# Kernel optimization log

Hardware: AMD Instinct MI355X
Metric: run time of the kernel (lower is better)

Reference implementation:

```python
import jax, jax.numpy as jnp
import numpy as np

CUTOFF = 5.0
CUTOFF_ANGLE = 3.5
N = 25000
E = 800000
EA = 300000
T = 1600000
NBASIS = 8          # default radial basis size (bessel)
NBASIS_ANG = 8
DIM = 256
DIM_SRC = 64
DIM_DST = 32
DIM_ANGLE = 8
NMAX_ANGLE = 4
SPECIES_DIM = 16
NSPEC = 50


def bessel_basis(r, rc, n):
    # sin(k*pi*r/rc)/r Bessel-type radial basis, k=1..n  -> [E, n]
    x = r[:, None]
    k = jnp.arange(1, n + 1, dtype=r.dtype)[None, :] * (np.pi / rc)
    return jnp.sqrt(2.0 / rc) * jnp.sin(k * x) / x


def tssr2(x):
    # two-sided smooth square-root activation (identity inside |x|<=1)
    ax = jnp.abs(x)
    return jnp.where(ax <= 1.0, x, jnp.sign(x) * (2.0 * jnp.sqrt(jnp.maximum(ax, 1.0)) - 1.0))


def setup_inputs() -> dict:
    key = jax.random.key(0)
    ks = jax.random.split(key, 24)
    species = jax.random.randint(ks[0], (N,), 1, 17)
    edge_src = jax.random.randint(ks[1], (E,), 0, N)
    edge_dst = jax.random.randint(ks[2], (E,), 0, N)
    distances = 0.5 + jax.random.uniform(ks[3], (E,)) * (CUTOFF - 0.5)
    switch = 0.5 + 0.5 * jnp.cos(np.pi * distances / CUTOFF)
    angles = jax.random.uniform(ks[4], (T,)) * np.pi
    angle_src = jax.random.randint(ks[5], (T,), 0, EA)
    angle_dst = jax.random.randint(ks[6], (T,), 0, EA)
    central_atom = jax.random.randint(ks[7], (T,), 0, N)
    distances_angle = 0.5 + jax.random.uniform(ks[8], (EA,)) * (CUTOFF_ANGLE - 0.5)
    switch_angle = 0.5 + 0.5 * jnp.cos(np.pi * distances_angle / CUTOFF_ANGLE)
    s = lambda k, sh, scale: jax.random.normal(k, sh, jnp.float32) * scale
    din0 = SPECIES_DIM + DIM_SRC + NBASIS * DIM_DST + (NMAX_ANGLE + 1) * DIM_ANGLE  # 376
    din1 = DIM + DIM_SRC + NBASIS * DIM_DST + (NMAX_ANGLE + 1) * DIM_ANGLE          # 616
    return {
        'species': species, 'edge_src': edge_src, 'edge_dst': edge_dst,
        'distances': distances, 'switch': switch,
        'angles': angles, 'angle_src': angle_src, 'angle_dst': angle_dst,
        'central_atom': central_atom, 'distances_angle': distances_angle,
        'switch_angle': switch_angle,
        'species_table': s(ks[9], (NSPEC, SPECIES_DIM), 1.0),
        'W_si0': s(ks[10], (SPECIES_DIM, DIM_SRC + DIM_DST), SPECIES_DIM ** -0.5),
        'W_si1': s(ks[11], (DIM, DIM_SRC + DIM_DST), DIM ** -0.5),
        'W_da0': s(ks[12], (NBASIS_ANG, DIM_ANGLE), NBASIS_ANG ** -0.5),
        'W_da1': s(ks[13], (NBASIS_ANG, DIM_ANGLE), NBASIS_ANG ** -0.5),
        'W_mix0': s(ks[14], (din0, DIM), din0 ** -0.5),
        'b_mix0': jnp.zeros((DIM,), jnp.float32),
        'W_mix1': s(ks[15], (din1, DIM), din1 ** -0.5),
        'b_mix1': jnp.zeros((DIM,), jnp.float32),
    }


def reference(species, edge_src, edge_dst, distances, switch, angles, angle_src,
              angle_dst, central_atom, distances_angle, switch_angle,
              species_table, W_si0, W_si1, W_da0, W_da1,
              W_mix0, b_mix0, W_mix1, b_mix1):
    n_atoms = species.shape[0]
    # species encoding (learned/random table lookup)
    xi = species_table[species]                                   # [N, 16]
    # radial embeddings, smoothly switched at cutoff
    rb = bessel_basis(distances, CUTOFF, NBASIS) * switch[:, None]            # [E, 8]
    rba = bessel_basis(distances_angle, CUTOFF_ANGLE, NBASIS_ANG) * switch_angle[:, None]  # [EA, 8]
    # fourier angular features cos(n*theta), n=0..nmax_angle
    nvec = jnp.arange(NMAX_ANGLE + 1, dtype=angles.dtype)[None, :]
    xa = jnp.cos(nvec * angles[:, None])                          # [T, 5]
    for W_si, W_da, W_mix, b_mix in ((W_si0, W_da0, W_mix0, b_mix0),
                                     (W_si1, W_da1, W_mix1, b_mix1)):
        s = xi @ W_si                                             # [N, 96]
        si, si_dst = s[:, :DIM_SRC], s[:, DIM_SRC:]
        # radial message passing: outer(radial_basis, neighbor features) -> scatter-add
        mij = (rb[:, :, None] * si_dst[edge_dst][:, None, :]).reshape(rb.shape[0], -1)  # [E, 256]
        mi = jax.ops.segment_sum(mij, edge_src, num_segments=n_atoms)                   # [N, 256]
        # angular triplet features: pairwise vectors combined per angle
        da = rba @ W_da                                           # [EA, 8]
        dij = da[angle_src] * da[angle_dst]                       # [T, 8]
        ang = (xa[:, :, None] * dij[:, None, :]).reshape(xa.shape[0], -1)               # [T, 40]
        ami = jax.ops.segment_sum(ang, central_atom, num_segments=n_atoms)              # [N, 40]
        # mixing network + tssr2 mixing activation, residual when shapes match
        ei = jnp.concatenate([xi, si, mi, ami], axis=-1)
        dxi = tssr2(ei @ W_mix + b_mix)
        xi = xi + dxi if xi.shape[-1] == dxi.shape[-1] else dxi
    return xi
```

## Files before the change

### kernel.cpp

```cpp
#include <hip/hip_runtime.h>
#include <hip/hip_bf16.h>

typedef __hip_bfloat16 bf16;
typedef __bf16 bf8 __attribute__((ext_vector_type(8)));
typedef float  f4  __attribute__((ext_vector_type(4)));

#define N_ATOMS 25000
#define NE      800000
#define NEA     300000
#define NT      1600000
#define APB     64
#define NBUK    ((N_ATOMS + APB - 1) / APB)

#define DIN0  376
#define DIN1  616
#define DINP0 384
#define DINP1 640

#define EBLK ((NE + 4095) / 4096)
#define TBLK ((NT + 4095) / 4096)

#define NFRAG0 ((DINP0 / 32) * 16 * 64)
#define NFRAG1 ((DINP1 / 32) * 16 * 64)
#define NFRAGS (8 * 6 * 64)

#define S0BLK ((N_ATOMS * 120 + 255) / 256)
#define DABLK ((NEA + 255) / 256)

#define MIBLK ((N_ATOMS + 1) / 2)

__device__ __forceinline__ float tssr2f(float x) {
    float ax = fabsf(x);
    return (ax <= 1.f) ? x : copysignf(2.f * __builtin_sqrtf(ax) - 1.f, x);
}

__device__ __forceinline__ unsigned short f2bf_rn(float v) {
    unsigned int b = __float_as_uint(v);
    b += 0x7FFF + ((b >> 16) & 1);
    return (unsigned short)(b >> 16);
}
__device__ __forceinline__ float bf2f(unsigned short u) {
    return __uint_as_float(((unsigned int)u) << 16);
}

__global__ __launch_bounds__(256) void k_bcount(const int* __restrict__ esrc,
                                                const int* __restrict__ cat,
                                                int* __restrict__ ebcnt,
                                                int* __restrict__ tbcnt) {
    __shared__ int h[NBUK];
    int t = threadIdx.x;
    for (int b = t; b < NBUK; b += 256) h[b] = 0;
    __syncthreads();
    bool isE = blockIdx.x < EBLK;
    const int* key = isE ? esrc : cat;
    int n = isE ? NE : NT;
    int base = (isE ? blockIdx.x : (blockIdx.x - EBLK)) * 4096;
#pragma unroll
    for (int k = 0; k < 16; k++) {
        int idx = base + k * 256 + t;
        if (idx < n) atomicAdd(&h[key[idx] >> 6], 1);
    }
    __syncthreads();
    int* g = isE ? ebcnt : tbcnt;
    for (int b = t; b < NBUK; b += 256)
        if (h[b]) atomicAdd(&g[b], h[b]);
}

__global__ __launch_bounds__(512) void k_scanB(const int* cnt0, int* off0, int* cur0,
                                               int* aoff0,
                                               const int* cnt1, int* off1, int* cur1,
                                               int* aoff1) {
    const int* cnt = blockIdx.x ? cnt1 : cnt0;
    int* off  = blockIdx.x ? off1 : off0;
    int* cur  = blockIdx.x ? cur1 : cur0;
    int* aoff = blockIdx.x ? aoff1 : aoff0;
    int nelem = blockIdx.x ? NT : NE;
    __shared__ int sh[512];
    int t = threadIdx.x;
    int v = (t < NBUK) ? cnt[t] : 0;
    sh[t] = v;
    __syncthreads();
    for (int d = 1; d < 512; d <<= 1) {
        int a = (t >= d) ? sh[t - d] : 0;
        __syncthreads();
        sh[t] += a;
        __syncthreads();
    }
    int excl = sh[t] - v;
    if (t <= NBUK) { off[t] = excl; if (t < NBUK) cur[t] = excl; }
    if (t == 0) aoff[N_ATOMS] = nelem;
}

__global__ __launch_bounds__(512) void k_binA2(const float* __restrict__ eA,
                                               const float* __restrict__ eB,
                                               const int* __restrict__ eC,
                                               const int* __restrict__ ekey,
                                               int* __restrict__ egcur,
                                               float4* __restrict__ ebuk,
                                               const float* __restrict__ tA,
                                               const int* __restrict__ tB,
                                               const int* __restrict__ tC,
                                               const int* __restrict__ tkey,
                                               int* __restrict__ tgcur,
                                               float4* __restrict__ tbuk) {
    __shared__ int cnt[NBUK];
    __shared__ int rbase[NBUK];
    int t = threadIdx.x;
    for (int b = t; b < NBUK; b += 512) cnt[b] = 0;
    __syncthreads();
    bool isE = blockIdx.x < EBLK;
    const int* key = isE ? ekey : tkey;
    int n = isE ? NE : NT;
    int* gcur = isE ? egcur : tgcur;
    float4* buk = isE ? ebuk : tbuk;
    int base = (isE ? blockIdx.x : (blockIdx.x - EBLK)) * 4096;
    float4 pay[8];
    int bk[8], off[8];
#pragma unroll
    for (int k = 0; k < 8; k++) {
        int idx = base + k * 512 + t;
        bk[k] = -1;
        if (idx < n) {
            float4 p;
            if (isE) {
                p.x = eA[idx];
                p.y = eB[idx];
                p.z = __int_as_float(eC[idx]);
            } else {
                p.x = __cosf(tA[idx]);
                p.y = __int_as_float(tB[idx]);
                p.z = __int_as_float(tC[idx]);
            }
            int ky = key[idx];
            p.w = __int_as_float(ky);
            pay[k] = p;
            bk[k] = ky >> 6;
            off[k] = atomicAdd(&cnt[bk[k]], 1);
        }
    }
    __syncthreads();
    for (int b = t; b < NBUK; b += 512)
        if (cnt[b]) rbase[b] = atomicAdd(&gcur[b], cnt[b]);
    __syncthreads();
#pragma unroll
    for (int k = 0; k < 8; k++)
        if (bk[k] >= 0) buk[rbase[bk[k]] + off[k]] = pay[k];
}

__global__ __launch_bounds__(256) void k_binB2(const int* __restrict__ ebkoff,
                                               const float4* __restrict__ ebuk,
                                               float* __restrict__ erb,
                                               int* __restrict__ edi,
                                               int* __restrict__ eoff,
                                               const int* __restrict__ tbkoff,
                                               const float4* __restrict__ tbuk,
                                               float4* __restrict__ tfin,
                                               int* __restrict__ toff) {
    bool isE = blockIdx.x < NBUK;
    int b = isE ? blockIdx.x : (blockIdx.x - NBUK);
    const int* bkoff = isE ? ebkoff : tbkoff;
    const float4* buk = isE ? ebuk : tbuk;
    int* aoff = isE ? eoff : toff;
    int lo = b * APB;
    int hi = min(lo + APB, N_ATOMS);
    __shared__ int cnt[APB];
    __shared__ int cur[APB];
    int t = threadIdx.x;
    if (t < APB) cnt[t] = 0;
    __syncthreads();
    int pbeg = bkoff[b], pend = bkoff[b + 1];
    for (int p = pbeg + t; p < pend; p += 256) {
        int a = __float_as_int(((const float*)(buk + p))[3]);
        atomicAdd(&cnt[a - lo], 1);
    }
    __syncthreads();
    if (t == 0) {
        int run = pbeg;
        for (int k = 0; k < hi - lo; k++) {
            cur[k] = run;
            aoff[lo + k] = run;
            run += cnt[k];
        }
    }
    __syncthreads();
    for (int p = pbeg + t; p < pend; p += 256) {
        float4 pay = buk[p];
        int a = __float_as_int(pay.w);
        int slot = atomicAdd(&cur[a - lo], 1);
        if (isE) {
            float d = pay.x, s = pay.y;
            float q = 0.6324555320f * s / d;
            float r[8];
#pragma unroll
            for (int n = 0; n < 8; n++)
                r[n] = q * __sinf((n + 1) * 0.6283185307f * d);
            *(float4*)&erb[(size_t)slot * 8]     = make_float4(r[0], r[1], r[2], r[3]);
            *(float4*)&erb[(size_t)slot * 8 + 4] = make_float4(r[4], r[5], r[6], r[7]);
            edi[slot] = __float_as_int(pay.z);
        } else {
            tfin[slot] = pay;
        }
    }
}

__device__ __forceinline__ void wprep_one(const float* __restrict__ W, bf8* __restrict__ Wf,
                                          int K, int N, int ntiles, int f) {
    int lane = f & 63;
    int ft = f >> 6;
    int tile = ft % ntiles;
    int chunk = ft / ntiles;
    int n = tile * 16 + (lane & 15);
    int kb = chunk * 32 + (lane >> 4) * 8;
    bf8 v;
#pragma unroll
    for (int j = 0; j < 8; j++) {
        int k = kb + j;
        v[j] = (__bf16)((k < K) ? W[k * N + n] : 0.f);
    }
    Wf[f] = v;
}

__global__ __launch_bounds__(256) void k_wprep3(const float* __restrict__ W0, bf8* __restrict__ Wf0,
                                                const float* __restrict__ W1, bf8* __restrict__ Wf1,
                                                const float* __restrict__ WS, bf8* __restrict__ WfS) {
    int f = blockIdx.x * 256 + threadIdx.x;
    if (f < NFRAG0) {
        wprep_one(W0, Wf0, DIN0, 256, 16, f);
    } else if (f < NFRAG0 + NFRAG1) {
        wprep_one(W1, Wf1, DIN1, 256, 16, f - NFRAG0);
    } else if (f < NFRAG0 + NFRAG1 + NFRAGS) {
        wprep_one(WS, WfS, 256, 96, 6, f - NFRAG0 - NFRAG1);
    }
}

__global__ __launch_bounds__(256) void k_pre(const int* __restrict__ sp,
                                             const float* __restrict__ table,
                                             const float* __restrict__ W,
                                             float* __restrict__ ei0,
                                             float* __restrict__ sd,
                                             const float* __restrict__ dist,
                                             const float* __restrict__ sw,
                                             const float* __restrict__ Wda0,
                                             const float* __restrict__ Wda1,
                                             unsigned short* __restrict__ dah0,
                                             unsigned short* __restrict__ dah1) {
    if ((int)blockIdx.x < S0BLK) {
        int idx = blockIdx.x * 256 + threadIdx.x;
        if (idx >= N_ATOMS * 120) return;
        int i = idx / 120;
        int c = idx - i * 120;
        if (c >= 112) {
            ei0[(size_t)i * DINP0 + 376 + (c - 112)] = 0.f;
            return;
        }
        int s = sp[i];
        if (c < 16) {
            ei0[(size_t)i * DINP0 + c] = table[s * 16 + c];
        } else {
            int cc = c - 16;
            float acc = 0.f;
#pragma unroll
            for (int k = 0; k < 16; k++)
                acc += table[s * 16 + k] * W[k * 96 + cc];
            if (cc < 64) ei0[(size_t)i * DINP0 + 16 + cc] = acc;
            else         sd[i * 32 + cc - 64]             = acc;
        }
    } else {
        int e = (blockIdx.x - S0BLK) * 256 + threadIdx.x;
        if (e >= NEA) return;
        float d = dist[e];
        float s = sw[e];
        float rb[8];
#pragma unroll
        for (int n = 0; n < 8; n++)
            rb[n] = 0.7559289460f * __sinf((n + 1) * 0.8975979010f * d) / d * s;
        unsigned short h0[8], h1[8];
#pragma unroll
        for (int c = 0; c < 8; c++) {
            float a0 = 0.f, a1 = 0.f;
#pragma unroll
            for (int n = 0; n < 8; n++) {
                a0 += rb[n] * Wda0[n * 8 + c];
                a1 += rb[n] * Wda1[n * 8 + c];
            }
            h0[c] = f2bf_rn(a0);
            h1[c] = f2bf_rn(a1);
        }
        *(uint4*)&dah0[e * 8] = *(uint4*)h0;
        *(uint4*)&dah1[e * 8] = *(uint4*)h1;
    }
}

__global__ __launch_bounds__(256) void k_s1(const float* __restrict__ ei1,
                                            const bf8* __restrict__ Wf,
                                            float* __restrict__ ei1o,
                                            float* __restrict__ sd) {
    __shared__ __align__(16) __bf16 Asg[4][64][8];
    int t = threadIdx.x;
    int w = t >> 6, lane = t & 63;
    int a0 = blockIdx.x * 64;

    int satom = a0 + (t >> 2);
    int k8 = (t & 3) * 8;
    const float* arow = &ei1[(size_t)satom * DINP1 + k8];
    bool aok = satom < N_ATOMS;
    int dw = (t >> 2) >> 4;
    int dl = ((t >> 2) & 15) | ((t & 3) << 4);
    __bf16* adst = &Asg[dw][dl][0];

    f4 acc[6];
#pragma unroll
    for (int j = 0; j < 6; j++) {
        f4 z = {0.f, 0.f, 0.f, 0.f};
        acc[j] = z;
    }

    for (int ch = 0; ch < 8; ch++) {
        float4 v0 = make_float4(0.f, 0.f, 0.f, 0.f);
        float4 v1 = make_float4(0.f, 0.f, 0.f, 0.f);
        if (aok) {
            v0 = *(const float4*)(arow + ch * 32);
            v1 = *(const float4*)(arow + ch * 32 + 4);
        }
        __syncthreads();
        adst[0] = (__bf16)v0.x; adst[1] = (__bf16)v0.y;
        adst[2] = (__bf16)v0.z; adst[3] = (__bf16)v0.w;
        adst[4] = (__bf16)v1.x; adst[5] = (__bf16)v1.y;
        adst[6] = (__bf16)v1.z; adst[7] = (__bf16)v1.w;
        __syncthreads();
        bf8 afr = *(const bf8*)&Asg[w][lane][0];
        const bf8* wp = &Wf[(ch * 6) * 64 + lane];
#pragma unroll
        for (int tn = 0; tn < 6; tn++) {
            bf8 b = wp[tn * 64];
            acc[tn] = __builtin_amdgcn_mfma_f32_16x16x32_bf16(afr, b, acc[tn], 0, 0, 0);
        }
    }

    int nlo = lane & 15, q = lane >> 4;
#pragma unroll
    for (int r = 0; r < 4; r++) {
        int atom = a0 + w * 16 + q * 4 + r;
        if (atom < N_ATOMS) {
#pragma unroll
            for (int tn = 0; tn < 6; tn++) {
                int col = tn * 16 + nlo;
                float v = acc[tn][r];
                if (col < 64) ei1o[(size_t)atom * DINP1 + 256 + col] = v;
                else          sd[atom * 32 + col - 64] = v;
            }
        }
    }
    for (int z = t; z < 64 * 24; z += 256) {
        int za = a0 + z / 24;
        if (za < N_ATOMS) ei1o[(size_t)za * DINP1 + 616 + z % 24] = 0.f;
    }
}

__device__ __forceinline__ void ami_win(const float4 twA, const unsigned short* __restrict__ dah,
                                        int lim, int jj, int c,
                                        float& a0, float& a1, float& a2, float& a3, float& a4) {
    int gmax = (lim + 7) >> 3;
    float sc = 0.f; unsigned short dA = 0, dB = 0;
    {
        sc = __shfl(twA.x, jj, 64);
        int ea = __float_as_int(__shfl(twA.y, jj, 64));
        int eb = __float_as_int(__shfl(twA.z, jj, 64));
        dA = dah[ea * 8 + c];
        dB = dah[eb * 8 + c];
    }
    for (int g = 0; g < gmax; g++) {
        float scN = 0.f; unsigned short dAN = 0, dBN = 0;
        if (g + 1 < gmax) {
            int sl = (g + 1) * 8 + jj;
            scN = __shfl(twA.x, sl, 64);
            int ea = __float_as_int(__shfl(twA.y, sl, 64));
            int eb = __float_as_int(__shfl(twA.z, sl, 64));
            dAN = dah[ea * 8 + c];
            dBN = dah[eb * 8 + c];
        }
        float dij = bf2f(dA) * bf2f(dB);
        dij = (g * 8 + jj < lim) ? dij : 0.f;
        float c1 = sc;
        float c2 = __builtin_fmaf(2.f * c1, c1, -1.f);
        float c3 = __builtin_fmaf(2.f * c1, c2, -c1);
        float c4 = __builtin_fmaf(2.f * c1, c3, -c2);
        a0 += dij;
        a1 = __builtin_fmaf(c1, dij, a1);
        a2 = __builtin_fmaf(c2, dij, a2);
        a3 = __builtin_fmaf(c3, dij, a3);
        a4 = __builtin_fmaf(c4, dij, a4);
        if (g + 1 < gmax) { sc = scN; dA = dAN; dB = dBN; }
    }
}

__global__ __launch_bounds__(256) void k_seg(const int* __restrict__ eoff,
                                             const float* __restrict__ erb,
                                             const int* __restrict__ edi,
                                             const float* __restrict__ sd,
                                             float* __restrict__ mo, int mstride,
                                             const int* __restrict__ toff,
                                             const float4* __restrict__ tpay,
                                             const unsigned short* __restrict__ dah,
                                             float* __restrict__ ao, int astride) {
    __shared__ float4 smi[2][64];
    __shared__ float  sam[2][5][8];
    int t = threadIdx.x;
    int wv = t >> 6, l = t & 63;
    int slot = wv >> 1;
    int p    = wv & 1;

    if ((int)blockIdx.x < MIBLK) {
        int i = blockIdx.x * 2 + slot;
        bool valid = (i < N_ATOMS);
        int beg = 0, end = 0;
        if (valid) { beg = eoff[i]; end = eoff[i + 1]; }
        int cnt = end - beg;
        int n = l >> 3, cb = (l & 7) * 4;
        float4 acc = make_float4(0.f, 0.f, 0.f, 0.f);

        if (cnt > 0) {
            int nG = (cnt + 7) >> 3;
            int h0 = (nG + 1) >> 1;
            int gbeg = p ? h0 : 0;
            int gend = p ? nG : h0;
            if (cnt <= 64) {
                int eWin = edi[beg + min(l, cnt - 1)];
                int cmax = end * 8 - 1;
                if (gbeg < gend) {
                    float cA = erb[min((beg + gbeg * 8) * 8 + l, cmax)];
                    for (int g = gbeg; g < gend; g++) {
                        int e8 = g * 8;
                        float4 v[8];
#pragma unroll
                        for (int j = 0; j < 8; j++) {
                            int eid = __shfl(eWin, e8 + j, 64);
                            v[j] = *(const float4*)&sd[eid * 32 + cb];
                        }
                        float cB = 0.f;
                        if (g + 1 < gend) cB = erb[min((beg + e8 + 8) * 8 + l, cmax)];
#pragma unroll
                        for (int j = 0; j < 8; j++) {
                            float r_ = __shfl(cA, j * 8 + n, 64);
                            r_ = (e8 + j < cnt) ? r_ : 0.f;
                            acc.x += r_ * v[j].x; acc.y += r_ * v[j].y;
                            acc.z += r_ * v[j].z; acc.w += r_ * v[j].w;
                        }
                        if (g + 1 < gend) cA = cB;
                    }
                }
            } else {
                const float* rp = erb + (size_t)beg * 8 + n;
                const int*   dp = edi + beg;
                for (int g = gbeg; g < gend; g++) {
                    int e8 = g * 8;
                    int m = cnt - e8;
#pragma unroll
                    for (int j = 0; j < 8; j++) {
                        int jj = min(j, m - 1);
                        float rb = rp[(e8 + jj) * 8];
                        int di = dp[e8 + jj];
                        if (j >= m) rb = 0.f;
                        float4 v = *(const float4*)&sd[di * 32 + cb];
                        acc.x += rb * v.x; acc.y += rb * v.y;
                        acc.z += rb * v.z; acc.w += rb * v.w;
                    }
                }
            }
        }

        if (p == 1) smi[slot][l] = acc;
        __syncthreads();
        if (valid && p == 0) {
            float4 o = smi[slot][l];
            acc.x += o.x; acc.y += o.y; acc.z += o.z; acc.w += o.w;
            *(float4*)&mo[(size_t)i * mstride + l * 4] = acc;
        }
    } else {
        int i = ((int)blockIdx.x - MIBLK) * 2 + slot;
        bool valid = (i < N_ATOMS);
        int beg = 0, end = 0;
        if (valid) { beg = toff[i]; end = toff[i + 1]; }
        int cnt = end - beg;
        int jj = l >> 3, c = l & 7;
        float a0 = 0.f, a1 = 0.f, a2 = 0.f, a3 = 0.f, a4 = 0.f;

        if (cnt > 0) {
            if (cnt <= 128) {
                int nG = (cnt + 7) >> 3;
                int h0 = (nG + 1) >> 1;
                int tb = p ? h0 * 8 : 0;
                int te = p ? cnt : min(h0 * 8, cnt);
                int mycnt = te - tb;
                if (mycnt > 0) {
                    float4 twA = tpay[beg + tb + min(l, mycnt - 1)];
                    ami_win(twA, dah, mycnt, jj, c, a0, a1, a2, a3, a4);
                }
            } else {
                int nW = (cnt + 63) >> 6;
                for (int W = p; W < nW; W += 2) {
                    int wbase = W * 64;
                    int rem = cnt - wbase;
                    int lim = min(rem, 64);
                    float4 twA = tpay[beg + wbase + min(l, rem - 1)];
                    ami_win(twA, dah, lim, jj, c, a0, a1, a2, a3, a4);
                }
            }
        }

#pragma unroll
        for (int msk = 8; msk <= 32; msk <<= 1) {
            a0 += __shfl_xor(a0, msk, 64);
            a1 += __shfl_xor(a1, msk, 64);
            a2 += __shfl_xor(a2, msk, 64);
            a3 += __shfl_xor(a3, msk, 64);
            a4 += __shfl_xor(a4, msk, 64);
        }
        if (p == 1 && l < 8) {
            sam[slot][0][l] = a0; sam[slot][1][l] = a1; sam[slot][2][l] = a2;
            sam[slot][3][l] = a3; sam[slot][4][l] = a4;
        }
        __syncthreads();
        if (valid && p == 0 && l < 8) {
            a0 += sam[slot][0][l]; a1 += sam[slot][1][l]; a2 += sam[slot][2][l];
            a3 += sam[slot][3][l]; a4 += sam[slot][4][l];
            float* o = &ao[(size_t)i * astride + c];
            o[0]  = a0;
            o[8]  = a1;
            o[16] = a2;
            o[24] = a3;
            o[32] = a4;
        }
    }
}

template <int LAYER>
__global__ __launch_bounds__(256) void k_gemm(const float* __restrict__ ei,
                                              const bf8* __restrict__ Wf,
                                              const float* __restrict__ bias,
                                              const float* __restrict__ skip,
                                              float* __restrict__ out) {
    constexpr int DINP = (LAYER == 0) ? DINP0 : DINP1;
    constexpr int NCH = DINP / 32;
    __shared__ __align__(16) __bf16 Asg[2][64][8];
    int t = threadIdx.x;
    int w = t >> 6, lane = t & 63;
    int a0 = blockIdx.x * 32;

    int f  = t * 4;
    int tA = f >> 9;
    int al = (f >> 3) & 63;
    int j0 = f & 7;
    int sm = al & 15, sq = al >> 4;
    int ga = a0 + tA * 16 + sm;
    const float* arow = &ei[(size_t)ga * DINP + sq * 8 + j0];
    __bf16* adst = &Asg[0][0][0] + f;
    bool aok = (ga < N_ATOMS);

    f4 acc[2][4];
#pragma unroll
    for (int i = 0; i < 2; i++)
#pragma unroll
        for (int j = 0; j < 4; j++) {
            f4 z = {0.f, 0.f, 0.f, 0.f};
            acc[i][j] = z;
        }

    for (int ch = 0; ch < NCH; ch++) {
        float4 v = make_float4(0.f, 0.f, 0.f, 0.f);
        if (aok) v = *(const float4*)(arow + ch * 32);
        __syncthreads();
        adst[0] = (__bf16)v.x; adst[1] = (__bf16)v.y;
        adst[2] = (__bf16)v.z; adst[3] = (__bf16)v.w;
        __syncthreads();
        bf8 afr0 = *(const bf8*)&Asg[0][lane][0];
        bf8 afr1 = *(const bf8*)&Asg[1][lane][0];
        const bf8* wp = &Wf[(ch * 16 + w * 4) * 64 + lane];
#pragma unroll
        for (int tn = 0; tn < 4; tn++) {
            bf8 b = wp[tn * 64];
            acc[0][tn] = __builtin_amdgcn_mfma_f32_16x16x32_bf16(afr0, b, acc[0][tn], 0, 0, 0);
            acc[1][tn] = __builtin_amdgcn_mfma_f32_16x16x32_bf16(afr1, b, acc[1][tn], 0, 0, 0);
        }
    }

    int nlo = lane & 15, q = lane >> 4;
#pragma unroll
    for (int tA2 = 0; tA2 < 2; tA2++) {
#pragma unroll
        for (int r = 0; r < 4; r++) {
            int atom = a0 + tA2 * 16 + q * 4 + r;
            if (atom < N_ATOMS) {
#pragma unroll
                for (int tn = 0; tn < 4; tn++) {
                    int col = w * 64 + tn * 16 + nlo;
                    float vv = tssr2f(acc[tA2][tn][r] + bias[col]);
                    if (LAYER == 0) {
                        out[(size_t)atom * DINP1 + col] = vv;
                    } else {
                        out[(size_t)atom * 256 + col] = vv + skip[(size_t)atom * DINP1 + col];
                    }
                }
            }
        }
    }
}

extern "C" void kernel_launch(void* const* d_in, const int* in_sizes, int n_in,
                              void* d_out, int out_size, void* d_ws, size_t ws_size,
                              hipStream_t stream) {
    const int*   species     = (const int*)d_in[0];
    const int*   edge_src    = (const int*)d_in[1];
    const int*   edge_dst    = (const int*)d_in[2];
    const float* distances   = (const float*)d_in[3];
    const float* sw          = (const float*)d_in[4];
    const float* angles      = (const float*)d_in[5];
    const int*   angle_src   = (const int*)d_in[6];
    const int*   angle_dst   = (const int*)d_in[7];
    const int*   central     = (const int*)d_in[8];
    const float* dist_a      = (const float*)d_in[9];
    const float* sw_a        = (const float*)d_in[10];
    const float* table       = (const float*)d_in[11];
    const float* W_si0       = (const float*)d_in[12];
    const float* W_si1       = (const float*)d_in[13];
    const float* W_da0       = (const float*)d_in[14];
    const float* W_da1       = (const float*)d_in[15];
    const float* W_mix0      = (const float*)d_in[16];
    const float* b_mix0      = (const float*)d_in[17];
    const float* W_mix1      = (const float*)d_in[18];
    const float* b_mix1      = (const float*)d_in[19];
    float* out = (float*)d_out;

    char* p = (char*)d_ws;
    auto alloc = [&](size_t bytes) {
        char* r = p;
        p += (bytes + 255) & ~(size_t)255;
        return (void*)r;
    };
    float*  ei0  = (float*)alloc((size_t)N_ATOMS * DINP0 * 4);
    float*  ei1  = (float*)alloc((size_t)N_ATOMS * DINP1 * 4);
    float*  sd   = (float*)alloc((size_t)N_ATOMS * 32 * 4);
    unsigned short* dah0 = (unsigned short*)alloc((size_t)NEA * 8 * 2);
    unsigned short* dah1 = (unsigned short*)alloc((size_t)NEA * 8 * 2);
    float*  erbf = (float*)alloc((size_t)NE * 8 * 4);
    int*    edi  = (int*)alloc((size_t)NE * 4);
    float4* tpay = (float4*)alloc((size_t)NT * 16);
    bf8*    Wf0  = (bf8*)alloc((size_t)NFRAG0 * 16);
    bf8*    Wf1  = (bf8*)alloc((size_t)NFRAG1 * 16);
    bf8*    WfS1 = (bf8*)alloc((size_t)NFRAGS * 16);
    int* eoff   = (int*)alloc((size_t)(N_ATOMS + 1) * 4);
    int* toff   = (int*)alloc((size_t)(N_ATOMS + 1) * 4);
    int* bcnt   = (int*)alloc((size_t)2 * NBUK * 4);
    int* ebkoff = (int*)alloc((size_t)(NBUK + 1) * 4);
    int* tbkoff = (int*)alloc((size_t)(NBUK + 1) * 4);
    int* gce    = (int*)alloc((size_t)NBUK * 4);
    int* gct    = (int*)alloc((size_t)NBUK * 4);
    (void)ws_size;
    int* ebcnt = bcnt;
    int* tbcnt = bcnt + NBUK;

    float4* tbuk = (float4*)ei1;
    float4* ebuk = (float4*)((char*)ei1 + (size_t)NT * 16);

    hipMemsetAsync(bcnt, 0, (size_t)2 * NBUK * 4, stream);

    k_wprep3<<<(NFRAG0 + NFRAG1 + NFRAGS + 255) / 256, 256, 0, stream>>>(
        W_mix0, Wf0, W_mix1, Wf1, W_si1, WfS1);

    k_bcount<<<EBLK + TBLK, 256, 0, stream>>>(edge_src, central, ebcnt, tbcnt);
    k_scanB<<<2, 512, 0, stream>>>(ebcnt, ebkoff, gce, eoff, tbcnt, tbkoff, gct, toff);

    k_binA2<<<EBLK + TBLK, 512, 0, stream>>>(
        distances, sw, edge_dst, edge_src, gce, ebuk,
        angles, angle_src, angle_dst, central, gct, tbuk);
    k_binB2<<<2 * NBUK, 256, 0, stream>>>(
        ebkoff, ebuk, erbf, edi, eoff,
        tbkoff, tbuk, tpay, toff);

    k_pre<<<S0BLK + DABLK, 256, 0, stream>>>(
        species, table, W_si0, ei0, sd,
        dist_a, sw_a, W_da0, W_da1, dah0, dah1);

    int gemm_grid = (N_ATOMS + 31) / 32;

    k_seg<<<2 * MIBLK, 256, 0, stream>>>(eoff, erbf, edi, sd, ei0 + 80, DINP0,
                                         toff, tpay, dah0, ei0 + 336, DINP0);
    k_gemm<0><<<gemm_grid, 256, 0, stream>>>(ei0, Wf0, b_mix0, nullptr, ei1);

    k_s1<<<(N_ATOMS + 63) / 64, 256, 0, stream>>>(ei1, WfS1, ei1, sd);
    k_seg<<<2 * MIBLK, 256, 0, stream>>>(eoff, erbf, edi, sd, ei1 + 320, DINP1,
                                         toff, tpay, dah1, ei1 + 576, DINP1);
    k_gemm<1><<<gemm_grid, 256, 0, stream>>>(ei1, Wf1, b_mix1, ei1, out);
}
```

Before: 417.6 us.

## Store intermediate per-atom feature buffers in bf16 instead of fp32

The concatenated per-atom feature buffers (ei0, ei1) are now written and read as bf16 rather than fp32. The seg, pre and s1 kernels round their outputs to bf16, and the GEMM kernels copy the bf16 words straight into shared memory instead of loading floats and converting. This is meant to roughly halve the memory traffic on these large intermediates, since the GEMM already consumed them as bf16. The k_seg block ordering is also swapped so that triplet (angular) blocks come before the radial message blocks, and the bucket scratch space is re-aliased into the smaller buffers. The trade-off is that the residual skip connection and stored features lose precision through bf16 rounding.

After: 412.2 us. Within noise of the previous version (-1.3%).

```diff
diff --git a/kernel.cpp b/kernel.cpp
--- a/kernel.cpp
+++ b/kernel.cpp
@@ -236,7 +236,7 @@
 __global__ __launch_bounds__(256) void k_pre(const int* __restrict__ sp,
                                              const float* __restrict__ table,
                                              const float* __restrict__ W,
-                                             float* __restrict__ ei0,
+                                             unsigned short* __restrict__ ei0,
                                              float* __restrict__ sd,
                                              const float* __restrict__ dist,
                                              const float* __restrict__ sw,
@@ -250,19 +250,19 @@
         int i = idx / 120;
         int c = idx - i * 120;
         if (c >= 112) {
-            ei0[(size_t)i * DINP0 + 376 + (c - 112)] = 0.f;
+            ei0[(size_t)i * DINP0 + 376 + (c - 112)] = 0;
             return;
         }
         int s = sp[i];
         if (c < 16) {
-            ei0[(size_t)i * DINP0 + c] = table[s * 16 + c];
+            ei0[(size_t)i * DINP0 + c] = f2bf_rn(table[s * 16 + c]);
         } else {
             int cc = c - 16;
             float acc = 0.f;
 #pragma unroll
             for (int k = 0; k < 16; k++)
                 acc += table[s * 16 + k] * W[k * 96 + cc];
-            if (cc < 64) ei0[(size_t)i * DINP0 + 16 + cc] = acc;
+            if (cc < 64) ei0[(size_t)i * DINP0 + 16 + cc] = f2bf_rn(acc);
             else         sd[i * 32 + cc - 64]             = acc;
         }
     } else {
@@ -291,9 +291,9 @@
     }
 }
 
-__global__ __launch_bounds__(256) void k_s1(const float* __restrict__ ei1,
+__global__ __launch_bounds__(256) void k_s1(const unsigned short* __restrict__ ei1,
                                             const bf8* __restrict__ Wf,
-                                            float* __restrict__ ei1o,
+                                            unsigned short* __restrict__ ei1o,
                                             float* __restrict__ sd) {
     __shared__ __align__(16) __bf16 Asg[4][64][8];
     int t = threadIdx.x;
@@ -302,7 +302,7 @@
 
     int satom = a0 + (t >> 2);
     int k8 = (t & 3) * 8;
-    const float* arow = &ei1[(size_t)satom * DINP1 + k8];
+    const unsigned short* arow = &ei1[(size_t)satom * DINP1 + k8];
     bool aok = satom < N_ATOMS;
     int dw = (t >> 2) >> 4;
     int dl = ((t >> 2) & 15) | ((t & 3) << 4);
@@ -316,17 +316,10 @@
     }
 
     for (int ch = 0; ch < 8; ch++) {
-        float4 v0 = make_float4(0.f, 0.f, 0.f, 0.f);
-        float4 v1 = make_float4(0.f, 0.f, 0.f, 0.f);
-        if (aok) {
-            v0 = *(const float4*)(arow + ch * 32);
-            v1 = *(const float4*)(arow + ch * 32 + 4);
-        }
-        __syncthreads();
-        adst[0] = (__bf16)v0.x; adst[1] = (__bf16)v0.y;
-        adst[2] = (__bf16)v0.z; adst[3] = (__bf16)v0.w;
-        adst[4] = (__bf16)v1.x; adst[5] = (__bf16)v1.y;
-        adst[6] = (__bf16)v1.z; adst[7] = (__bf16)v1.w;
+        uint4 v = make_uint4(0, 0, 0, 0);
+        if (aok) v = *(const uint4*)(arow + ch * 32);
+        __syncthreads();
+        *(uint4*)adst = v;
         __syncthreads();
         bf8 afr = *(const bf8*)&Asg[w][lane][0];
         const bf8* wp = &Wf[(ch * 6) * 64 + lane];
@@ -346,14 +339,14 @@
             for (int tn = 0; tn < 6; tn++) {
                 int col = tn * 16 + nlo;
                 float v = acc[tn][r];
-                if (col < 64) ei1o[(size_t)atom * DINP1 + 256 + col] = v;
+                if (col < 64) ei1o[(size_t)atom * DINP1 + 256 + col] = f2bf_rn(v);
                 else          sd[atom * 32 + col - 64] = v;
             }
         }
     }
     for (int z = t; z < 64 * 24; z += 256) {
         int za = a0 + z / 24;
-        if (za < N_ATOMS) ei1o[(size_t)za * DINP1 + 616 + z % 24] = 0.f;
+        if (za < N_ATOMS) ei1o[(size_t)za * DINP1 + 616 + z % 24] = 0;
     }
 }
 
@@ -398,11 +391,11 @@
                                              const float* __restrict__ erb,
                                              const int* __restrict__ edi,
                                              const float* __restrict__ sd,
-                                             float* __restrict__ mo, int mstride,
+                                             unsigned short* __restrict__ mo, int mstride,
                                              const int* __restrict__ toff,
                                              const float4* __restrict__ tpay,
                                              const unsigned short* __restrict__ dah,
-                                             float* __restrict__ ao, int astride) {
+                                             unsigned short* __restrict__ ao, int astride) {
     __shared__ float4 smi[2][64];
     __shared__ float  sam[2][5][8];
     int t = threadIdx.x;
@@ -412,72 +405,6 @@
 
     if ((int)blockIdx.x < MIBLK) {
         int i = blockIdx.x * 2 + slot;
-        bool valid = (i < N_ATOMS);
-        int beg = 0, end = 0;
-        if (valid) { beg = eoff[i]; end = eoff[i + 1]; }
-        int cnt = end - beg;
-        int n = l >> 3, cb = (l & 7) * 4;
-        float4 acc = make_float4(0.f, 0.f, 0.f, 0.f);
-
-        if (cnt > 0) {
-            int nG = (cnt + 7) >> 3;
-            int h0 = (nG + 1) >> 1;
-            int gbeg = p ? h0 : 0;
-            int gend = p ? nG : h0;
-            if (cnt <= 64) {
-                int eWin = edi[beg + min(l, cnt - 1)];
-                int cmax = end * 8 - 1;
-                if (gbeg < gend) {
-                    float cA = erb[min((beg + gbeg * 8) * 8 + l, cmax)];
-                    for (int g = gbeg; g < gend; g++) {
-                        int e8 = g * 8;
-                        float4 v[8];
-#pragma unroll
-                        for (int j = 0; j < 8; j++) {
-                            int eid = __shfl(eWin, e8 + j, 64);
-                            v[j] = *(const float4*)&sd[eid * 32 + cb];
-                        }
-                        float cB = 0.f;
-                        if (g + 1 < gend) cB = erb[min((beg + e8 + 8) * 8 + l, cmax)];
-#pragma unroll
-                        for (int j = 0; j < 8; j++) {
-                            float r_ = __shfl(cA, j * 8 + n, 64);
-                            r_ = (e8 + j < cnt) ? r_ : 0.f;
-                            acc.x += r_ * v[j].x; acc.y += r_ * v[j].y;
-                            acc.z += r_ * v[j].z; acc.w += r_ * v[j].w;
-                        }
-                        if (g + 1 < gend) cA = cB;
-                    }
-                }
-            } else {
-                const float* rp = erb + (size_t)beg * 8 + n;
-                const int*   dp = edi + beg;
-                for (int g = gbeg; g < gend; g++) {
-                    int e8 = g * 8;
-                    int m = cnt - e8;
-#pragma unroll
-                    for (int j = 0; j < 8; j++) {
-                        int jj = min(j, m - 1);
-                        float rb = rp[(e8 + jj) * 8];
-                        int di = dp[e8 + jj];
-                        if (j >= m) rb = 0.f;
-                        float4 v = *(const float4*)&sd[di * 32 + cb];
-                        acc.x += rb * v.x; acc.y += rb * v.y;
-                        acc.z += rb * v.z; acc.w += rb * v.w;
-                    }
-                }
-            }
-        }
-
-        if (p == 1) smi[slot][l] = acc;
-        __syncthreads();
-        if (valid && p == 0) {
-            float4 o = smi[slot][l];
-            acc.x += o.x; acc.y += o.y; acc.z += o.z; acc.w += o.w;
-            *(float4*)&mo[(size_t)i * mstride + l * 4] = acc;
-        }
-    } else {
-        int i = ((int)blockIdx.x - MIBLK) * 2 + slot;
         bool valid = (i < N_ATOMS);
         int beg = 0, end = 0;
         if (valid) { beg = toff[i]; end = toff[i + 1]; }
@@ -524,22 +451,91 @@
         if (valid && p == 0 && l < 8) {
             a0 += sam[slot][0][l]; a1 += sam[slot][1][l]; a2 += sam[slot][2][l];
             a3 += sam[slot][3][l]; a4 += sam[slot][4][l];
-            float* o = &ao[(size_t)i * astride + c];
-            o[0]  = a0;
-            o[8]  = a1;
-            o[16] = a2;
-            o[24] = a3;
-            o[32] = a4;
+            unsigned short* o = &ao[(size_t)i * astride + c];
+            o[0]  = f2bf_rn(a0);
+            o[8]  = f2bf_rn(a1);
+            o[16] = f2bf_rn(a2);
+            o[24] = f2bf_rn(a3);
+            o[32] = f2bf_rn(a4);
+        }
+    } else {
+        int i = ((int)blockIdx.x - MIBLK) * 2 + slot;
+        bool valid = (i < N_ATOMS);
+        int beg = 0, end = 0;
+        if (valid) { beg = eoff[i]; end = eoff[i + 1]; }
+        int cnt = end - beg;
+        int n = l >> 3, cb = (l & 7) * 4;
+        float4 acc = make_float4(0.f, 0.f, 0.f, 0.f);
+
+        if (cnt > 0) {
+            int nG = (cnt + 7) >> 3;
+            int h0 = (nG + 1) >> 1;
+            int gbeg = p ? h0 : 0;
+            int gend = p ? nG : h0;
+            if (cnt <= 64) {
+                int eWin = edi[beg + min(l, cnt - 1)];
+                int cmax = end * 8 - 1;
+                if (gbeg < gend) {
+                    float cA = erb[min((beg + gbeg * 8) * 8 + l, cmax)];
+                    for (int g = gbeg; g < gend; g++) {
+                        int e8 = g * 8;
+                        float4 v[8];
+#pragma unroll
+                        for (int j = 0; j < 8; j++) {
+                            int eid = __shfl(eWin, e8 + j, 64);
+                            v[j] = *(const float4*)&sd[eid * 32 + cb];
+                        }
+                        float cB = 0.f;
+                        if (g + 1 < gend) cB = erb[min((beg + e8 + 8) * 8 + l, cmax)];
+#pragma unroll
+                        for (int j = 0; j < 8; j++) {
+                            float r_ = __shfl(cA, j * 8 + n, 64);
+                            r_ = (e8 + j < cnt) ? r_ : 0.f;
+                            acc.x += r_ * v[j].x; acc.y += r_ * v[j].y;
+                            acc.z += r_ * v[j].z; acc.w += r_ * v[j].w;
+                        }
+                        if (g + 1 < gend) cA = cB;
+                    }
+                }
+            } else {
+                const float* rp = erb + (size_t)beg * 8 + n;
+                const int*   dp = edi + beg;
+                for (int g = gbeg; g < gend; g++) {
+                    int e8 = g * 8;
+                    int m = cnt - e8;
+#pragma unroll
+                    for (int j = 0; j < 8; j++) {
+                        int jj = min(j, m - 1);
+                        float rb = rp[(e8 + jj) * 8];
+                        int di = dp[e8 + jj];
+                        if (j >= m) rb = 0.f;
+                        float4 v = *(const float4*)&sd[di * 32 + cb];
+                        acc.x += rb * v.x; acc.y += rb * v.y;
+                        acc.z += rb * v.z; acc.w += rb * v.w;
+                    }
+                }
+            }
+        }
+
+        if (p == 1) smi[slot][l] = acc;
+        __syncthreads();
+        if (valid && p == 0) {
+            float4 o = smi[slot][l];
+            acc.x += o.x; acc.y += o.y; acc.z += o.z; acc.w += o.w;
+            ushort4 pk = make_ushort4(f2bf_rn(acc.x), f2bf_rn(acc.y),
+                                      f2bf_rn(acc.z), f2bf_rn(acc.w));
+            *(ushort4*)&mo[(size_t)i * mstride + l * 4] = pk;
         }
     }
 }
 
 template <int LAYER>
-__global__ __launch_bounds__(256) void k_gemm(const float* __restrict__ ei,
+__global__ __launch_bounds__(256) void k_gemm(const unsigned short* __restrict__ ei,
                                               const bf8* __restrict__ Wf,
                                               const float* __restrict__ bias,
-                                              const float* __restrict__ skip,
-                                              float* __restrict__ out) {
+                                              const unsigned short* __restrict__ skip,
+                                              float* __restrict__ outf,
+                                              unsigned short* __restrict__ outb) {
     constexpr int DINP = (LAYER == 0) ? DINP0 : DINP1;
     constexpr int NCH = DINP / 32;
     __shared__ __align__(16) __bf16 Asg[2][64][8];
@@ -553,7 +549,7 @@
     int j0 = f & 7;
     int sm = al & 15, sq = al >> 4;
     int ga = a0 + tA * 16 + sm;
-    const float* arow = &ei[(size_t)ga * DINP + sq * 8 + j0];
+    const unsigned short* arow = &ei[(size_t)ga * DINP + sq * 8 + j0];
     __bf16* adst = &Asg[0][0][0] + f;
     bool aok = (ga < N_ATOMS);
 
@@ -567,11 +563,10 @@
         }
 
     for (int ch = 0; ch < NCH; ch++) {
-        float4 v = make_float4(0.f, 0.f, 0.f, 0.f);
-        if (aok) v = *(const float4*)(arow + ch * 32);
-        __syncthreads();
-        adst[0] = (__bf16)v.x; adst[1] = (__bf16)v.y;
-        adst[2] = (__bf16)v.z; adst[3] = (__bf16)v.w;
+        uint2 v = make_uint2(0, 0);
+        if (aok) v = *(const uint2*)(arow + ch * 32);
+        __syncthreads();
+        *(uint2*)adst = v;
         __syncthreads();
         bf8 afr0 = *(const bf8*)&Asg[0][lane][0];
         bf8 afr1 = *(const bf8*)&Asg[1][lane][0];
@@ -596,9 +591,10 @@
                     int col = w * 64 + tn * 16 + nlo;
                     float vv = tssr2f(acc[tA2][tn][r] + bias[col]);
                     if (LAYER == 0) {
-                        out[(size_t)atom * DINP1 + col] = vv;
+                        outb[(size_t)atom * DINP1 + col] = f2bf_rn(vv);
                     } else {
-                        out[(size_t)atom * 256 + col] = vv + skip[(size_t)atom * DINP1 + col];
+                        outf[(size_t)atom * 256 + col] =
+                            vv + bf2f(skip[(size_t)atom * DINP1 + col]);
                     }
                 }
             }
@@ -637,8 +633,8 @@
         p += (bytes + 255) & ~(size_t)255;
         return (void*)r;
     };
-    float*  ei0  = (float*)alloc((size_t)N_ATOMS * DINP0 * 4);
-    float*  ei1  = (float*)alloc((size_t)N_ATOMS * DINP1 * 4);
+    unsigned short* ei0 = (unsigned short*)alloc((size_t)N_ATOMS * DINP0 * 2);
+    unsigned short* ei1 = (unsigned short*)alloc((size_t)N_ATOMS * DINP1 * 2);
     float*  sd   = (float*)alloc((size_t)N_ATOMS * 32 * 4);
     unsigned short* dah0 = (unsigned short*)alloc((size_t)NEA * 8 * 2);
     unsigned short* dah1 = (unsigned short*)alloc((size_t)NEA * 8 * 2);
@@ -659,8 +655,8 @@
     int* ebcnt = bcnt;
     int* tbcnt = bcnt + NBUK;
 
+    float4* ebuk = (float4*)ei0;
     float4* tbuk = (float4*)ei1;
-    float4* ebuk = (float4*)((char*)ei1 + (size_t)NT * 16);
 
     hipMemsetAsync(bcnt, 0, (size_t)2 * NBUK * 4, stream);
 
@@ -685,10 +681,10 @@
 
     k_seg<<<2 * MIBLK, 256, 0, stream>>>(eoff, erbf, edi, sd, ei0 + 80, DINP0,
                                          toff, tpay, dah0, ei0 + 336, DINP0);
-    k_gemm<0><<<gemm_grid, 256, 0, stream>>>(ei0, Wf0, b_mix0, nullptr, ei1);
+    k_gemm<0><<<gemm_grid, 256, 0, stream>>>(ei0, Wf0, b_mix0, nullptr, nullptr, ei1);
 
     k_s1<<<(N_ATOMS + 63) / 64, 256, 0, stream>>>(ei1, WfS1, ei1, sd);
     k_seg<<<2 * MIBLK, 256, 0, stream>>>(eoff, erbf, edi, sd, ei1 + 320, DINP1,
                                          toff, tpay, dah1, ei1 + 576, DINP1);
-    k_gemm<1><<<gemm_grid, 256, 0, stream>>>(ei1, Wf1, b_mix1, ei1, out);
-}
+    k_gemm<1><<<gemm_grid, 256, 0, stream>>>(ei1, Wf1, b_mix1, ei1, out, nullptr);
+}
```
